# Performance work log

Measured on AMD Instinct MI355X. Metric: run time of the kernel, lower is better.

## Reference

```python
import jax, jax.numpy as jnp
import numpy as np

B = 64
RX, RZ, RX_, RZ_ = 32, 16, 16, 8
TN = 1
STRIDE = 2
IN_DIM, OUT_DIM = 256, 512
KEY_DIM, H, ATTN_RATIO = 32, 8, 2
D = ATTN_RATIO * KEY_DIM            # per-head value dim = 64
DH = D * H                          # 512
NH_KD = KEY_DIM * H                 # 256
N = RX * RX + TN * RZ * RZ          # 1280 tokens (search + template)
N_ = RX_ * RX_ + TN * RZ_ * RZ_     # 320 subsampled query tokens
SCALE = KEY_DIM ** -0.5
EPS = 1e-5


def linear_bn(x, W, gamma, beta):
    # Linear (no bias) followed by BatchNorm1d in training mode over (B*N, C)
    y = jnp.einsum('bnc,oc->bno', x, W)
    m = y.mean(axis=(0, 1))
    v = y.var(axis=(0, 1))  # biased variance, as torch BN uses for normalization
    return (y - m) * jax.lax.rsqrt(v + EPS) * gamma + beta


def subsample(x):
    # stride-subsample the search-region tokens and each template's tokens
    b, n, c = x.shape
    parts = [x[:, :RX * RX].reshape(b, RX, RX, c)[:, ::STRIDE, ::STRIDE].reshape(b, -1, c)]
    for i in range(TN):
        s = RX * RX + i * RZ * RZ
        z = x[:, s:s + RZ * RZ].reshape(b, RZ, RZ, c)[:, ::STRIDE, ::STRIDE].reshape(b, -1, c)
        parts.append(z)
    return jnp.concatenate(parts, axis=1)


def setup_inputs() -> dict:
    key = jax.random.key(0)
    ks = jax.random.split(key, 4)
    return {
        'x': jax.random.normal(ks[0], (B, N, IN_DIM), dtype=jnp.float32),
        'W_kv': jax.random.normal(ks[1], (NH_KD + DH, IN_DIM), dtype=jnp.float32) * 0.02,
        'g_kv': jnp.ones((NH_KD + DH,), jnp.float32),
        'b_kv': jnp.zeros((NH_KD + DH,), jnp.float32),
        'W_q': jax.random.normal(ks[2], (NH_KD, IN_DIM), dtype=jnp.float32) * 0.02,
        'g_q': jnp.ones((NH_KD,), jnp.float32),
        'b_q': jnp.zeros((NH_KD,), jnp.float32),
        'W_p': jax.random.normal(ks[3], (OUT_DIM, DH), dtype=jnp.float32) * 0.02,
        'g_p': jnp.ones((OUT_DIM,), jnp.float32),
        'b_p': jnp.zeros((OUT_DIM,), jnp.float32),
    }


def reference(x, W_kv, g_kv, b_kv, W_q, g_q, b_q, W_p, g_p, b_p):
    b = x.shape[0]
    # fused KV projection + BN, then split into per-head K and V
    kv = linear_bn(x, W_kv, g_kv, b_kv).reshape(b, N, H, KEY_DIM + D)
    k = kv[..., :KEY_DIM].transpose(0, 2, 1, 3)   # [B,H,N,key_dim]
    v = kv[..., KEY_DIM:].transpose(0, 2, 1, 3)   # [B,H,N,d]
    # Q: subsample tokens, then Linear_BN
    q = linear_bn(subsample(x), W_q, g_q, b_q).reshape(b, N_, H, KEY_DIM).transpose(0, 2, 1, 3)
    attn = jax.nn.softmax(jnp.einsum('bhqd,bhkd->bhqk', q, k) * SCALE, axis=-1)
    o = jnp.einsum('bhqk,bhkd->bhqd', attn, v).transpose(0, 2, 1, 3).reshape(b, N_, DH)
    return linear_bn(jax.nn.hard_swish(o), W_p, g_p, b_p)
```

## Files before the change

### kernel.cpp

```cpp
#include <hip/hip_runtime.h>
#include <hip/hip_bf16.h>
#include <math.h>

#define EPSF 1e-5f
#define SCALEF 0.17677669529663687f
#define LOG2E 1.4426950408889634f

typedef unsigned short u16;
typedef unsigned int u32;
typedef __attribute__((ext_vector_type(8))) short bf16x8;
typedef __attribute__((ext_vector_type(4))) float f32x4;

__device__ __forceinline__ float b2f(u16 u) {
    union { unsigned int i; float f; } v; v.i = ((unsigned int)u) << 16; return v.f;
}
__device__ __forceinline__ u16 f2b(float f) {
    union { float f; unsigned int i; } v; v.f = f;
    unsigned int x = v.i;
    return (u16)((x + 0x7fffu + ((x >> 16) & 1u)) >> 16);
}
__device__ __forceinline__ float fexp2(float x) {
#if __has_builtin(__builtin_amdgcn_exp2f)
    return __builtin_amdgcn_exp2f(x);
#else
    return exp2f(x);
#endif
}
__device__ __forceinline__ u32 cvtpk_bf16(float lo, float hi) {
    u32 r;
    asm("v_cvt_pk_bf16_f32 %0, %1, %2" : "=v"(r) : "v"(lo), "v"(hi));
    return r;
}
__device__ __forceinline__ void gload_lds16(const u16* __restrict__ g, u16* l) {
    __builtin_amdgcn_global_load_lds(
        (const __attribute__((address_space(1))) void*)g,
        (__attribute__((address_space(3))) void*)l, 16, 0, 0);
}

__global__ void convert_f32_bf16(const float* __restrict__ src, u16* __restrict__ dst, int n4) {
    int i = blockIdx.x * 256 + threadIdx.x;
    if (i >= n4) return;
    float4 v = ((const float4*)src)[i];
    ushort4 o;
    o.x = f2b(v.x); o.y = f2b(v.y); o.z = f2b(v.z); o.w = f2b(v.w);
    ((ushort4*)dst)[i] = o;
}

__global__ void gather_sub_bf16(const u16* __restrict__ xb, u16* __restrict__ xsub, int n8) {
    int i = blockIdx.x * 256 + threadIdx.x;
    if (i >= n8) return;
    int e = i << 3;
    int row = e >> 8;
    int col = e & 255;
    int b = row / 320;
    int t = row - b * 320;
    int n;
    if (t < 256) n = ((t >> 4) << 6) + ((t & 15) << 1);
    else { int tt = t - 256; n = 1024 + ((tt >> 3) << 5) + ((tt & 7) << 1); }
    *(int4*)(xsub + e) = *(const int4*)(xb + ((size_t)(b * 1280 + n)) * 256 + col);
}

template<int OUT_F32>
__global__ __launch_bounds__(256) void gemm_bt(const u16* __restrict__ A, const u16* __restrict__ Bw,
                                               void* __restrict__ Cv, int M, int N, int K,
                                               float* __restrict__ sums) {
    __shared__ u16 As[128 * 32];
    __shared__ u16 Bs[128 * 32];
    __shared__ float sumbuf[4][64][2];
    const int tid = threadIdx.x;
    const int wave = tid >> 6, lane = tid & 63;
    const int quad = lane >> 4, lc = lane & 15;
    const int wr = wave >> 1, wc = wave & 1;
    const int m0 = blockIdx.y * 128, n0 = blockIdx.x * 128;

    const int srow = (wave << 5) + (lane >> 2);
    const int scol = (lane & 3) << 3;
    u16* ldsA0 = As + ((wave << 5) + 0) * 32;
    u16* ldsA1 = As + ((wave << 5) + 16) * 32;
    u16* ldsB0 = Bs + ((wave << 5) + 0) * 32;
    u16* ldsB1 = Bs + ((wave << 5) + 16) * 32;
    const u16* gA0 = A  + (size_t)(m0 + srow) * K + scol;
    const u16* gA1 = A  + (size_t)(m0 + srow + 16) * K + scol;
    const u16* gB0 = Bw + (size_t)(n0 + srow) * K + scol;
    const u16* gB1 = Bw + (size_t)(n0 + srow + 16) * K + scol;

    f32x4 acc[4][4];
#pragma unroll
    for (int i = 0; i < 4; ++i)
#pragma unroll
        for (int j = 0; j < 4; ++j) acc[i][j] = (f32x4){0.f, 0.f, 0.f, 0.f};

    for (int k0 = 0; k0 < K; k0 += 32) {
        __syncthreads();
        gload_lds16(gA0 + k0, ldsA0);
        gload_lds16(gA1 + k0, ldsA1);
        gload_lds16(gB0 + k0, ldsB0);
        gload_lds16(gB1 + k0, ldsB1);
        asm volatile("s_waitcnt vmcnt(0)" ::: "memory");
        __syncthreads();
        bf16x8 af[4], bfr[4];
#pragma unroll
        for (int mi = 0; mi < 4; ++mi) af[mi]  = *(const bf16x8*)&As[(wr * 64 + mi * 16 + lc) * 32 + quad * 8];
#pragma unroll
        for (int ni = 0; ni < 4; ++ni) bfr[ni] = *(const bf16x8*)&Bs[(wc * 64 + ni * 16 + lc) * 32 + quad * 8];
#pragma unroll
        for (int mi = 0; mi < 4; ++mi)
#pragma unroll
            for (int ni = 0; ni < 4; ++ni)
                acc[mi][ni] = __builtin_amdgcn_mfma_f32_16x16x32_bf16(af[mi], bfr[ni], acc[mi][ni], 0, 0, 0);
    }
    float ps[4], ps2[4];
#pragma unroll
    for (int ni = 0; ni < 4; ++ni) { ps[ni] = 0.f; ps2[ni] = 0.f; }
#pragma unroll
    for (int mi = 0; mi < 4; ++mi)
#pragma unroll
        for (int ni = 0; ni < 4; ++ni)
#pragma unroll
            for (int r = 0; r < 4; ++r) {
                int row = m0 + wr * 64 + mi * 16 + quad * 4 + r;
                int cn  = n0 + wc * 64 + ni * 16 + lc;
                float v = acc[mi][ni][r];
                ps[ni] += v; ps2[ni] += v * v;
                if (OUT_F32) ((float*)Cv)[(size_t)row * N + cn] = v;
                else         ((u16*)Cv)[(size_t)row * N + cn] = f2b(v);
            }
#pragma unroll
    for (int ni = 0; ni < 4; ++ni) {
        ps[ni]  += __shfl_xor(ps[ni], 16);  ps[ni]  += __shfl_xor(ps[ni], 32);
        ps2[ni] += __shfl_xor(ps2[ni], 16); ps2[ni] += __shfl_xor(ps2[ni], 32);
    }
    if (quad == 0) {
#pragma unroll
        for (int ni = 0; ni < 4; ++ni) {
            sumbuf[wave][ni * 16 + lc][0] = ps[ni];
            sumbuf[wave][ni * 16 + lc][1] = ps2[ni];
        }
    }
    __syncthreads();
    {
        int which = tid & 1, idx = (tid >> 1) & 63, wcg = tid >> 7;
        int channel = n0 + wcg * 64 + idx;
        float v = sumbuf[wcg][idx][which] + sumbuf[wcg + 2][idx][which];
        int rep = blockIdx.y & 7;
        atomicAdd(&sums[(rep * 2 + which) * N + channel], v);
    }
}

__global__ void finalize_bn(const float* __restrict__ sum2, const float* __restrict__ g,
                            const float* __restrict__ beta, int cols, float inv_n, float scale,
                            float* __restrict__ AB) {
    int c = blockIdx.x * 256 + threadIdx.x;
    if (c >= cols) return;
    float s = 0.f, s2 = 0.f;
#pragma unroll
    for (int r = 0; r < 8; ++r) {
        s  += sum2[(r * 2 + 0) * cols + c];
        s2 += sum2[(r * 2 + 1) * cols + c];
    }
    float m = s * inv_n;
    float var = s2 * inv_n - m * m;
    float a = g[c] * rsqrtf(var + EPSF) * scale;
    AB[c] = a;
    AB[cols + c] = beta[c] * scale - m * a;
}

__global__ __launch_bounds__(256) void normalize_kv(const u16* __restrict__ kv, const float* __restrict__ AB,
                                                    u16* __restrict__ Kn, u16* __restrict__ Vtn) {
    __shared__ u16 Vs[64 * 66];
    const int h = blockIdx.x, nt = blockIdx.y, b = blockIdx.z;
    const int bh = b * 8 + h;
    const int tid = threadIdx.x;
    {
        int tok = tid >> 2, dk = (tid & 3) << 3;
        size_t src = ((size_t)(b * 1280 + nt * 64 + tok)) * 768 + h * 96 + dk;
        union { int4 v; u16 u[8]; } ld; ld.v = *(const int4*)(kv + src);
        union { int4 v; u16 u[8]; } st;
#pragma unroll
        for (int j = 0; j < 8; ++j) {
            int c = h * 96 + dk + j;
            st.u[j] = f2b(b2f(ld.u[j]) * AB[c] + AB[768 + c]);
        }
        int g = tok >> 5, kk = tok & 31;
        int rowp = nt * 64 + g * 32 + ((kk & 4) << 2) + ((kk >> 3) << 2) + (kk & 3);
        *(int4*)(Kn + ((size_t)bh * 1280 + rowp) * 32 + dk) = st.v;
    }
#pragma unroll
    for (int half = 0; half < 2; ++half) {
        int t = (tid >> 3) + half * 32;
        int dv = (tid & 7) << 3;
        size_t src = ((size_t)(b * 1280 + nt * 64 + t)) * 768 + h * 96 + 32 + dv;
        union { int4 v; u16 u[8]; } ld; ld.v = *(const int4*)(kv + src);
#pragma unroll
        for (int j = 0; j < 8; ++j) {
            int c = h * 96 + 32 + dv + j;
            Vs[(dv + j) * 66 + t] = f2b(b2f(ld.u[j]) * AB[c] + AB[768 + c]);
        }
    }
    __syncthreads();
#pragma unroll
    for (int half = 0; half < 2; ++half) {
        int d = (tid >> 3) + half * 32;
        int tc = (tid & 7) << 3;
        union { int4 v; u16 u[8]; } st;
#pragma unroll
        for (int j = 0; j < 8; ++j) st.u[j] = Vs[d * 66 + tc + j];
        *(int4*)(Vtn + ((size_t)bh * 64 + d) * 1280 + nt * 64 + tc) = st.v;
    }
}

__global__ __launch_bounds__(256, 2) void attn_kernel4(const u16* __restrict__ Kn, const u16* __restrict__ Vtn,
                                                       const u16* __restrict__ q_raw, const float* __restrict__ ABq,
                                                       u16* __restrict__ o_act) {
    const int tid = threadIdx.x;
    const int wave = tid >> 6, lane = tid & 63;
    const int quad = lane >> 4, lc = lane & 15;
    const int h = blockIdx.x, b = blockIdx.y;
    const int bh = b * 8 + h;

    float qa[8], qb[8];
#pragma unroll
    for (int j = 0; j < 8; ++j) { int c = h * 32 + quad * 8 + j; qa[j] = ABq[c]; qb[j] = ABq[256 + c]; }
    bf16x8 qf[5];
#pragma unroll
    for (int j = 0; j < 5; ++j) {
        const u16* qs = q_raw + ((size_t)(b * 320 + j * 64 + wave * 16 + lc)) * 256 + h * 32 + quad * 8;
        union { int4 v; u16 u[8]; } ld; ld.v = *(const int4*)qs;
        union { bf16x8 v; u16 u[8]; } st;
#pragma unroll
        for (int jj = 0; jj < 8; ++jj) st.u[jj] = f2b(b2f(ld.u[jj]) * qa[jj] + qb[jj]);
        qf[j] = st.v;
    }

    const u16* Kp = Kn + (size_t)bh * 1280 * 32 + lc * 32 + quad * 8;
    const u16* Vp = Vtn + (size_t)bh * 64 * 1280 + lc * 1280 + quad * 8;

    f32x4 acc[5][4];
#pragma unroll
    for (int j = 0; j < 5; ++j)
#pragma unroll
        for (int i = 0; i < 4; ++i) acc[j][i] = (f32x4){0.f, 0.f, 0.f, 0.f};
    float lsum[5];
#pragma unroll
    for (int j = 0; j < 5; ++j) lsum[j] = 0.f;

    const f32x4 z = (f32x4){0.f, 0.f, 0.f, 0.f};
    for (int kc = 0; kc < 1280; kc += 32) {
        bf16x8 kfA = *(const bf16x8*)(Kp + kc * 32);
        bf16x8 kfB = *(const bf16x8*)(Kp + kc * 32 + 512);
        bf16x8 vf0 = *(const bf16x8*)(Vp + kc);
        bf16x8 vf1 = *(const bf16x8*)(Vp + 16 * 1280 + kc);
        bf16x8 vf2 = *(const bf16x8*)(Vp + 32 * 1280 + kc);
        bf16x8 vf3 = *(const bf16x8*)(Vp + 48 * 1280 + kc);
        f32x4 s0[5], s1[5];
#pragma unroll
        for (int j = 0; j < 5; ++j) {
            s0[j] = __builtin_amdgcn_mfma_f32_16x16x32_bf16(kfA, qf[j], z, 0, 0, 0);
            s1[j] = __builtin_amdgcn_mfma_f32_16x16x32_bf16(kfB, qf[j], z, 0, 0, 0);
        }
#pragma unroll
        for (int j = 0; j < 5; ++j) {
            float p0 = fexp2(s0[j][0]);
            float p1 = fexp2(s0[j][1]);
            float p2 = fexp2(s0[j][2]);
            float p3 = fexp2(s0[j][3]);
            float p4 = fexp2(s1[j][0]);
            float p5 = fexp2(s1[j][1]);
            float p6 = fexp2(s1[j][2]);
            float p7 = fexp2(s1[j][3]);
            lsum[j] += ((p0 + p1) + (p2 + p3)) + ((p4 + p5) + (p6 + p7));
            union { u32 w[4]; bf16x8 v; } pf;
            pf.w[0] = cvtpk_bf16(p0, p1);
            pf.w[1] = cvtpk_bf16(p2, p3);
            pf.w[2] = cvtpk_bf16(p4, p5);
            pf.w[3] = cvtpk_bf16(p6, p7);
            acc[j][0] = __builtin_amdgcn_mfma_f32_16x16x32_bf16(vf0, pf.v, acc[j][0], 0, 0, 0);
            acc[j][1] = __builtin_amdgcn_mfma_f32_16x16x32_bf16(vf1, pf.v, acc[j][1], 0, 0, 0);
            acc[j][2] = __builtin_amdgcn_mfma_f32_16x16x32_bf16(vf2, pf.v, acc[j][2], 0, 0, 0);
            acc[j][3] = __builtin_amdgcn_mfma_f32_16x16x32_bf16(vf3, pf.v, acc[j][3], 0, 0, 0);
        }
    }
#pragma unroll
    for (int j = 0; j < 5; ++j) {
        float l = lsum[j];
        l += __shfl_xor(l, 16);
        l += __shfl_xor(l, 32);
        float inv = 1.f / l;
        int qrow = b * 320 + j * 64 + wave * 16 + lc;
        u16* dst = o_act + (size_t)qrow * 512 + h * 64 + quad * 4;
#pragma unroll
        for (int nt = 0; nt < 4; ++nt) {
            ushort4 st;
#pragma unroll
            for (int r = 0; r < 4; ++r) {
                float o = acc[j][nt][r] * inv;
                float hs = o * fminf(fmaxf(o + 3.f, 0.f), 6.f) * (1.f / 6.f);
                ((u16*)&st)[r] = f2b(hs);
            }
            *(ushort4*)(dst + nt * 16) = st;
        }
    }
}

__global__ void bn_apply_out(const float* __restrict__ praw, const float* __restrict__ ABp,
                             float* __restrict__ out, int n4) {
    int i = blockIdx.x * 256 + threadIdx.x;
    if (i >= n4) return;
    int e = i << 2;
    int c = e & 511;
    float4 v = ((const float4*)praw)[i];
    float4 o;
    o.x = v.x * ABp[c]     + ABp[512 + c];
    o.y = v.y * ABp[c + 1] + ABp[512 + c + 1];
    o.z = v.z * ABp[c + 2] + ABp[512 + c + 2];
    o.w = v.w * ABp[c + 3] + ABp[512 + c + 3];
    ((float4*)out)[i] = o;
}

extern "C" void kernel_launch(void* const* d_in, const int* in_sizes, int n_in,
                              void* d_out, int out_size, void* d_ws, size_t ws_size,
                              hipStream_t stream) {
    const float* x   = (const float*)d_in[0];
    const float* Wkv = (const float*)d_in[1];
    const float* gkv = (const float*)d_in[2];
    const float* bkv = (const float*)d_in[3];
    const float* Wq  = (const float*)d_in[4];
    const float* gq  = (const float*)d_in[5];
    const float* bq  = (const float*)d_in[6];
    const float* Wp  = (const float*)d_in[7];
    const float* gp  = (const float*)d_in[8];
    const float* bp  = (const float*)d_in[9];
    float* out = (float*)d_out;

    char* ws = (char*)d_ws;
    size_t off = 0;
    auto alloc = [&](size_t bytes) -> void* {
        void* p = ws + off;
        off += (bytes + 255) & ~(size_t)255;
        return p;
    };
    u16*   kv_raw = (u16*)alloc(81920ull * 768 * 2);
    u16*   q_raw  = (u16*)alloc(20480ull * 256 * 2);
    void*  slot1  = alloc(81920ull * 256 * 2);
    u16*   x_b    = (u16*)slot1;
    u16*   K_norm = (u16*)slot1;
    float* p_raw  = (float*)slot1;
    void*  slot2  = alloc(20480ull * 512 * 2);
    u16*   xsub_b = (u16*)slot2;
    u16*   o_act  = (u16*)slot2;
    u16*   Vt_norm = (u16*)alloc(512ull * 64 * 1280 * 2);
    u16*   Wkv_b  = (u16*)alloc(768ull * 256 * 2);
    u16*   Wq_b   = (u16*)alloc(256ull * 256 * 2);
    u16*   Wp_b   = (u16*)alloc(512ull * 512 * 2);
    float* sums_kv = (float*)alloc(8 * 2 * 768 * sizeof(float));
    float* sums_q  = (float*)alloc(8 * 2 * 256 * sizeof(float));
    float* sums_p  = (float*)alloc(8 * 2 * 512 * sizeof(float));
    float* ABkv = (float*)alloc(1536 * sizeof(float));
    float* ABq  = (float*)alloc(512 * sizeof(float));
    float* ABp  = (float*)alloc(1024 * sizeof(float));

    dim3 blk(256);
    hipMemsetAsync(sums_kv, 0, 8 * 2 * (768 + 256 + 512) * sizeof(float), stream);

    convert_f32_bf16<<<20480, blk, 0, stream>>>(x,   x_b,   5242880);
    convert_f32_bf16<<<192,   blk, 0, stream>>>(Wkv, Wkv_b, 49152);
    convert_f32_bf16<<<64,    blk, 0, stream>>>(Wq,  Wq_b,  16384);
    convert_f32_bf16<<<256,   blk, 0, stream>>>(Wp,  Wp_b,  65536);
    gather_sub_bf16<<<2560,   blk, 0, stream>>>(x_b, xsub_b, 655360);

    gemm_bt<0><<<dim3(6, 640), blk, 0, stream>>>(x_b, Wkv_b, kv_raw, 81920, 768, 256, sums_kv);
    gemm_bt<0><<<dim3(2, 160), blk, 0, stream>>>(xsub_b, Wq_b, q_raw, 20480, 256, 256, sums_q);

    finalize_bn<<<3, blk, 0, stream>>>(sums_kv, gkv, bkv, 768, 1.f / 81920.f, 1.f, ABkv);
    finalize_bn<<<1, blk, 0, stream>>>(sums_q,  gq,  bq,  256, 1.f / 20480.f, SCALEF * LOG2E, ABq);

    normalize_kv<<<dim3(8, 20, 64), blk, 0, stream>>>(kv_raw, ABkv, K_norm, Vt_norm);

    attn_kernel4<<<dim3(8, 64), blk, 0, stream>>>(K_norm, Vt_norm, q_raw, ABq, o_act);

    gemm_bt<1><<<dim3(4, 160), blk, 0, stream>>>(o_act, Wp_b, p_raw, 20480, 512, 512, sums_p);
    finalize_bn<<<2, blk, 0, stream>>>(sums_p, gp, bp, 512, 1.f / 20480.f, 1.f, ABp);

    bn_apply_out<<<10240, blk, 0, stream>>>(p_raw, ABp, out, 2621440);
}
```

Before: 398.1 us.

## Fold KV BatchNorm into attention and write K/Vt layouts from the GEMM epilogue

Removes the separate normalize_kv pass. The KV weight rows are permuted so the GEMM epilogue writes raw K, in its permuted row order, and transposed V straight to their attention layouts. The K BN scale is folded into the Q scale; its shift only adds a per-query constant that softmax cancels. The V BN affine is applied after softmax normalization, which is valid because the attention weights sum to one. The GEMM also gains a double-buffered LDS prefetch of the next K tile. The tradeoff is strided 8-byte V-transpose stores in the epilogue and wider-stride K loads in attention.

```diff
diff --git a/kernel.cpp b/kernel.cpp
--- a/kernel.cpp
+++ b/kernel.cpp
@@ -44,6 +44,13 @@
     ushort4 o;
     o.x = f2b(v.x); o.y = f2b(v.y); o.z = f2b(v.z); o.w = f2b(v.w);
     ((ushort4*)dst)[i] = o;
+}
+
+__global__ void convert_wkv_perm(const float* __restrict__ W, u16* __restrict__ out) {
+    int r = blockIdx.x, cl = threadIdx.x;
+    int src = (r < 256) ? ((r >> 5) * 96 + (r & 31))
+                        : (((r - 256) >> 6) * 96 + 32 + ((r - 256) & 63));
+    out[r * 256 + cl] = f2b(W[src * 256 + cl]);
 }
 
 __global__ void gather_sub_bf16(const u16* __restrict__ xb, u16* __restrict__ xsub, int n8) {
@@ -60,12 +67,13 @@
     *(int4*)(xsub + e) = *(const int4*)(xb + ((size_t)(b * 1280 + n)) * 256 + col);
 }
 
-template<int OUT_F32>
+template<int MODE>
 __global__ __launch_bounds__(256) void gemm_bt(const u16* __restrict__ A, const u16* __restrict__ Bw,
-                                               void* __restrict__ Cv, int M, int N, int K,
+                                               void* __restrict__ Cv, void* __restrict__ C2v,
+                                               int M, int N, int K,
                                                float* __restrict__ sums) {
-    __shared__ u16 As[128 * 32];
-    __shared__ u16 Bs[128 * 32];
+    __shared__ u16 As[2][128 * 32];
+    __shared__ u16 Bs[2][128 * 32];
     __shared__ float sumbuf[4][64][2];
     const int tid = threadIdx.x;
     const int wave = tid >> 6, lane = tid & 63;
@@ -75,10 +83,7 @@
 
     const int srow = (wave << 5) + (lane >> 2);
     const int scol = (lane & 3) << 3;
-    u16* ldsA0 = As + ((wave << 5) + 0) * 32;
-    u16* ldsA1 = As + ((wave << 5) + 16) * 32;
-    u16* ldsB0 = Bs + ((wave << 5) + 0) * 32;
-    u16* ldsB1 = Bs + ((wave << 5) + 16) * 32;
+    const int ldsoff = (wave << 5) * 32;
     const u16* gA0 = A  + (size_t)(m0 + srow) * K + scol;
     const u16* gA1 = A  + (size_t)(m0 + srow + 16) * K + scol;
     const u16* gB0 = Bw + (size_t)(n0 + srow) * K + scol;
@@ -90,25 +95,37 @@
 #pragma unroll
         for (int j = 0; j < 4; ++j) acc[i][j] = (f32x4){0.f, 0.f, 0.f, 0.f};
 
+    auto STAGE = [&](int buf, int k0) {
+        gload_lds16(gA0 + k0, &As[buf][ldsoff]);
+        gload_lds16(gA1 + k0, &As[buf][ldsoff + 16 * 32]);
+        gload_lds16(gB0 + k0, &Bs[buf][ldsoff]);
+        gload_lds16(gB1 + k0, &Bs[buf][ldsoff + 16 * 32]);
+    };
+
+    STAGE(0, 0);
+    int cur = 0;
     for (int k0 = 0; k0 < K; k0 += 32) {
-        __syncthreads();
-        gload_lds16(gA0 + k0, ldsA0);
-        gload_lds16(gA1 + k0, ldsA1);
-        gload_lds16(gB0 + k0, ldsB0);
-        gload_lds16(gB1 + k0, ldsB1);
-        asm volatile("s_waitcnt vmcnt(0)" ::: "memory");
-        __syncthreads();
+        if (k0 + 32 < K) {
+            STAGE(cur ^ 1, k0 + 32);
+            asm volatile("s_waitcnt vmcnt(4)" ::: "memory");
+        } else {
+            asm volatile("s_waitcnt vmcnt(0)" ::: "memory");
+        }
+        __builtin_amdgcn_s_barrier();
         bf16x8 af[4], bfr[4];
 #pragma unroll
-        for (int mi = 0; mi < 4; ++mi) af[mi]  = *(const bf16x8*)&As[(wr * 64 + mi * 16 + lc) * 32 + quad * 8];
-#pragma unroll
-        for (int ni = 0; ni < 4; ++ni) bfr[ni] = *(const bf16x8*)&Bs[(wc * 64 + ni * 16 + lc) * 32 + quad * 8];
+        for (int mi = 0; mi < 4; ++mi) af[mi]  = *(const bf16x8*)&As[cur][(wr * 64 + mi * 16 + lc) * 32 + quad * 8];
+#pragma unroll
+        for (int ni = 0; ni < 4; ++ni) bfr[ni] = *(const bf16x8*)&Bs[cur][(wc * 64 + ni * 16 + lc) * 32 + quad * 8];
 #pragma unroll
         for (int mi = 0; mi < 4; ++mi)
 #pragma unroll
             for (int ni = 0; ni < 4; ++ni)
                 acc[mi][ni] = __builtin_amdgcn_mfma_f32_16x16x32_bf16(af[mi], bfr[ni], acc[mi][ni], 0, 0, 0);
-    }
+        __builtin_amdgcn_s_barrier();
+        cur ^= 1;
+    }
+
     float ps[4], ps2[4];
 #pragma unroll
     for (int ni = 0; ni < 4; ++ni) { ps[ni] = 0.f; ps2[ni] = 0.f; }
@@ -118,13 +135,53 @@
         for (int ni = 0; ni < 4; ++ni)
 #pragma unroll
             for (int r = 0; r < 4; ++r) {
-                int row = m0 + wr * 64 + mi * 16 + quad * 4 + r;
-                int cn  = n0 + wc * 64 + ni * 16 + lc;
                 float v = acc[mi][ni][r];
                 ps[ni] += v; ps2[ni] += v * v;
-                if (OUT_F32) ((float*)Cv)[(size_t)row * N + cn] = v;
-                else         ((u16*)Cv)[(size_t)row * N + cn] = f2b(v);
             }
+
+    if (MODE == 0 || MODE == 1) {
+#pragma unroll
+        for (int mi = 0; mi < 4; ++mi)
+#pragma unroll
+            for (int ni = 0; ni < 4; ++ni)
+#pragma unroll
+                for (int r = 0; r < 4; ++r) {
+                    int row = m0 + wr * 64 + mi * 16 + quad * 4 + r;
+                    int cn  = n0 + wc * 64 + ni * 16 + lc;
+                    float v = acc[mi][ni][r];
+                    if (MODE == 1) ((float*)Cv)[(size_t)row * N + cn] = v;
+                    else           ((u16*)Cv)[(size_t)row * N + cn] = f2b(v);
+                }
+    } else if (n0 < 256) {
+        u16* Kr = (u16*)Cv;
+#pragma unroll
+        for (int mi = 0; mi < 4; ++mi)
+#pragma unroll
+            for (int r = 0; r < 4; ++r) {
+                int t = m0 + wr * 64 + mi * 16 + quad * 4 + r;
+                int kk = t & 31;
+                int pr = (t & ~31) + ((kk & 4) << 2) + ((kk >> 3) << 2) + (kk & 3);
+#pragma unroll
+                for (int ni = 0; ni < 4; ++ni) {
+                    int c = n0 + wc * 64 + ni * 16 + lc;
+                    Kr[(size_t)pr * 256 + c] = f2b(acc[mi][ni][r]);
+                }
+            }
+    } else {
+        u16* Vt = (u16*)C2v;
+#pragma unroll
+        for (int mi = 0; mi < 4; ++mi)
+#pragma unroll
+            for (int ni = 0; ni < 4; ++ni) {
+                int cp = n0 - 256 + wc * 64 + ni * 16 + lc;
+                int t0 = m0 + wr * 64 + mi * 16 + quad * 4;
+                uint2 w;
+                w.x = cvtpk_bf16(acc[mi][ni][0], acc[mi][ni][1]);
+                w.y = cvtpk_bf16(acc[mi][ni][2], acc[mi][ni][3]);
+                *(uint2*)(Vt + (size_t)cp * 81920 + t0) = w;
+            }
+    }
+
 #pragma unroll
     for (int ni = 0; ni < 4; ++ni) {
         ps[ni]  += __shfl_xor(ps[ni], 16);  ps[ni]  += __shfl_xor(ps[ni], 32);
@@ -149,7 +206,7 @@
 
 __global__ void finalize_bn(const float* __restrict__ sum2, const float* __restrict__ g,
                             const float* __restrict__ beta, int cols, float inv_n, float scale,
-                            float* __restrict__ AB) {
+                            float* __restrict__ AB, int kvperm) {
     int c = blockIdx.x * 256 + threadIdx.x;
     if (c >= cols) return;
     float s = 0.f, s2 = 0.f;
@@ -158,69 +215,36 @@
         s  += sum2[(r * 2 + 0) * cols + c];
         s2 += sum2[(r * 2 + 1) * cols + c];
     }
+    int src = c;
+    if (kvperm) {
+        src = (c < 256) ? ((c >> 5) * 96 + (c & 31))
+                        : (((c - 256) >> 6) * 96 + 32 + ((c - 256) & 63));
+    }
     float m = s * inv_n;
     float var = s2 * inv_n - m * m;
-    float a = g[c] * rsqrtf(var + EPSF) * scale;
+    float a = g[src] * rsqrtf(var + EPSF) * scale;
     AB[c] = a;
-    AB[cols + c] = beta[c] * scale - m * a;
-}
-
-__global__ __launch_bounds__(256) void normalize_kv(const u16* __restrict__ kv, const float* __restrict__ AB,
-                                                    u16* __restrict__ Kn, u16* __restrict__ Vtn) {
-    __shared__ u16 Vs[64 * 66];
-    const int h = blockIdx.x, nt = blockIdx.y, b = blockIdx.z;
-    const int bh = b * 8 + h;
-    const int tid = threadIdx.x;
-    {
-        int tok = tid >> 2, dk = (tid & 3) << 3;
-        size_t src = ((size_t)(b * 1280 + nt * 64 + tok)) * 768 + h * 96 + dk;
-        union { int4 v; u16 u[8]; } ld; ld.v = *(const int4*)(kv + src);
-        union { int4 v; u16 u[8]; } st;
-#pragma unroll
-        for (int j = 0; j < 8; ++j) {
-            int c = h * 96 + dk + j;
-            st.u[j] = f2b(b2f(ld.u[j]) * AB[c] + AB[768 + c]);
-        }
-        int g = tok >> 5, kk = tok & 31;
-        int rowp = nt * 64 + g * 32 + ((kk & 4) << 2) + ((kk >> 3) << 2) + (kk & 3);
-        *(int4*)(Kn + ((size_t)bh * 1280 + rowp) * 32 + dk) = st.v;
-    }
-#pragma unroll
-    for (int half = 0; half < 2; ++half) {
-        int t = (tid >> 3) + half * 32;
-        int dv = (tid & 7) << 3;
-        size_t src = ((size_t)(b * 1280 + nt * 64 + t)) * 768 + h * 96 + 32 + dv;
-        union { int4 v; u16 u[8]; } ld; ld.v = *(const int4*)(kv + src);
-#pragma unroll
-        for (int j = 0; j < 8; ++j) {
-            int c = h * 96 + 32 + dv + j;
-            Vs[(dv + j) * 66 + t] = f2b(b2f(ld.u[j]) * AB[c] + AB[768 + c]);
-        }
-    }
-    __syncthreads();
-#pragma unroll
-    for (int half = 0; half < 2; ++half) {
-        int d = (tid >> 3) + half * 32;
-        int tc = (tid & 7) << 3;
-        union { int4 v; u16 u[8]; } st;
-#pragma unroll
-        for (int j = 0; j < 8; ++j) st.u[j] = Vs[d * 66 + tc + j];
-        *(int4*)(Vtn + ((size_t)bh * 64 + d) * 1280 + nt * 64 + tc) = st.v;
-    }
-}
-
-__global__ __launch_bounds__(256, 2) void attn_kernel4(const u16* __restrict__ Kn, const u16* __restrict__ Vtn,
-                                                       const u16* __restrict__ q_raw, const float* __restrict__ ABq,
+    AB[cols + c] = beta[src] * scale - m * a;
+}
+
+__global__ __launch_bounds__(256, 2) void attn_kernel5(const u16* __restrict__ Kr, const u16* __restrict__ Vt,
+                                                       const u16* __restrict__ q_raw,
+                                                       const float* __restrict__ ABq,
+                                                       const float* __restrict__ ABkv,
                                                        u16* __restrict__ o_act) {
     const int tid = threadIdx.x;
     const int wave = tid >> 6, lane = tid & 63;
     const int quad = lane >> 4, lc = lane & 15;
     const int h = blockIdx.x, b = blockIdx.y;
-    const int bh = b * 8 + h;
 
     float qa[8], qb[8];
 #pragma unroll
-    for (int j = 0; j < 8; ++j) { int c = h * 32 + quad * 8 + j; qa[j] = ABq[c]; qb[j] = ABq[256 + c]; }
+    for (int j = 0; j < 8; ++j) {
+        int c = h * 32 + quad * 8 + j;
+        float ak = ABkv[c];
+        qa[j] = ABq[c] * ak;
+        qb[j] = ABq[256 + c] * ak;
+    }
     bf16x8 qf[5];
 #pragma unroll
     for (int j = 0; j < 5; ++j) {
@@ -232,8 +256,8 @@
         qf[j] = st.v;
     }
 
-    const u16* Kp = Kn + (size_t)bh * 1280 * 32 + lc * 32 + quad * 8;
-    const u16* Vp = Vtn + (size_t)bh * 64 * 1280 + lc * 1280 + quad * 8;
+    const u16* Kp = Kr + (size_t)b * 1280 * 256 + (size_t)lc * 256 + h * 32 + quad * 8;
+    const u16* Vp = Vt + ((size_t)(h * 64 + lc)) * 81920 + b * 1280 + quad * 8;
 
     f32x4 acc[5][4];
 #pragma unroll
@@ -246,12 +270,12 @@
 
     const f32x4 z = (f32x4){0.f, 0.f, 0.f, 0.f};
     for (int kc = 0; kc < 1280; kc += 32) {
-        bf16x8 kfA = *(const bf16x8*)(Kp + kc * 32);
-        bf16x8 kfB = *(const bf16x8*)(Kp + kc * 32 + 512);
+        bf16x8 kfA = *(const bf16x8*)(Kp + (size_t)kc * 256);
+        bf16x8 kfB = *(const bf16x8*)(Kp + (size_t)(kc + 16) * 256);
         bf16x8 vf0 = *(const bf16x8*)(Vp + kc);
-        bf16x8 vf1 = *(const bf16x8*)(Vp + 16 * 1280 + kc);
-        bf16x8 vf2 = *(const bf16x8*)(Vp + 32 * 1280 + kc);
-        bf16x8 vf3 = *(const bf16x8*)(Vp + 48 * 1280 + kc);
+        bf16x8 vf1 = *(const bf16x8*)(Vp + (size_t)16 * 81920 + kc);
+        bf16x8 vf2 = *(const bf16x8*)(Vp + (size_t)32 * 81920 + kc);
+        bf16x8 vf3 = *(const bf16x8*)(Vp + (size_t)48 * 81920 + kc);
         f32x4 s0[5], s1[5];
 #pragma unroll
         for (int j = 0; j < 5; ++j) {
@@ -280,6 +304,13 @@
             acc[j][3] = __builtin_amdgcn_mfma_f32_16x16x32_bf16(vf3, pf.v, acc[j][3], 0, 0, 0);
         }
     }
+    float av[16], bv[16];
+#pragma unroll
+    for (int t = 0; t < 16; ++t) {
+        int cv = 256 + h * 64 + (t >> 2) * 16 + quad * 4 + (t & 3);
+        av[t] = ABkv[cv];
+        bv[t] = ABkv[768 + cv];
+    }
 #pragma unroll
     for (int j = 0; j < 5; ++j) {
         float l = lsum[j];
@@ -293,7 +324,7 @@
             ushort4 st;
 #pragma unroll
             for (int r = 0; r < 4; ++r) {
-                float o = acc[j][nt][r] * inv;
+                float o = av[nt * 4 + r] * (acc[j][nt][r] * inv) + bv[nt * 4 + r];
                 float hs = o * fminf(fmaxf(o + 3.f, 0.f), 6.f) * (1.f / 6.f);
                 ((u16*)&st)[r] = f2b(hs);
             }
@@ -339,16 +370,15 @@
         off += (bytes + 255) & ~(size_t)255;
         return p;
     };
-    u16*   kv_raw = (u16*)alloc(81920ull * 768 * 2);
-    u16*   q_raw  = (u16*)alloc(20480ull * 256 * 2);
     void*  slot1  = alloc(81920ull * 256 * 2);
     u16*   x_b    = (u16*)slot1;
-    u16*   K_norm = (u16*)slot1;
     float* p_raw  = (float*)slot1;
+    u16*   K_raw  = (u16*)alloc(81920ull * 256 * 2);
+    u16*   Vt_raw = (u16*)alloc(512ull * 81920 * 2);
+    u16*   q_raw  = (u16*)alloc(20480ull * 256 * 2);
     void*  slot2  = alloc(20480ull * 512 * 2);
     u16*   xsub_b = (u16*)slot2;
     u16*   o_act  = (u16*)slot2;
-    u16*   Vt_norm = (u16*)alloc(512ull * 64 * 1280 * 2);
     u16*   Wkv_b  = (u16*)alloc(768ull * 256 * 2);
     u16*   Wq_b   = (u16*)alloc(256ull * 256 * 2);
     u16*   Wp_b   = (u16*)alloc(512ull * 512 * 2);
@@ -363,23 +393,21 @@
     hipMemsetAsync(sums_kv, 0, 8 * 2 * (768 + 256 + 512) * sizeof(float), stream);
 
     convert_f32_bf16<<<20480, blk, 0, stream>>>(x,   x_b,   5242880);
-    convert_f32_bf16<<<192,   blk, 0, stream>>>(Wkv, Wkv_b, 49152);
+    convert_wkv_perm<<<768,   blk, 0, stream>>>(Wkv, Wkv_b);
     convert_f32_bf16<<<64,    blk, 0, stream>>>(Wq,  Wq_b,  16384);
     convert_f32_bf16<<<256,   blk, 0, stream>>>(Wp,  Wp_b,  65536);
     gather_sub_bf16<<<2560,   blk, 0, stream>>>(x_b, xsub_b, 655360);
 
-    gemm_bt<0><<<dim3(6, 640), blk, 0, stream>>>(x_b, Wkv_b, kv_raw, 81920, 768, 256, sums_kv);
-    gemm_bt<0><<<dim3(2, 160), blk, 0, stream>>>(xsub_b, Wq_b, q_raw, 20480, 256, 256, sums_q);
-
-    finalize_bn<<<3, blk, 0, stream>>>(sums_kv, gkv, bkv, 768, 1.f / 81920.f, 1.f, ABkv);
-    finalize_bn<<<1, blk, 0, stream>>>(sums_q,  gq,  bq,  256, 1.f / 20480.f, SCALEF * LOG2E, ABq);
-
-    normalize_kv<<<dim3(8, 20, 64), blk, 0, stream>>>(kv_raw, ABkv, K_norm, Vt_norm);
-
-    attn_kernel4<<<dim3(8, 64), blk, 0, stream>>>(K_norm, Vt_norm, q_raw, ABq, o_act);
-
-    gemm_bt<1><<<dim3(4, 160), blk, 0, stream>>>(o_act, Wp_b, p_raw, 20480, 512, 512, sums_p);
-    finalize_bn<<<2, blk, 0, stream>>>(sums_p, gp, bp, 512, 1.f / 20480.f, 1.f, ABp);
+    gemm_bt<2><<<dim3(6, 640), blk, 0, stream>>>(x_b, Wkv_b, K_raw, Vt_raw, 81920, 768, 256, sums_kv);
+    gemm_bt<0><<<dim3(2, 160), blk, 0, stream>>>(xsub_b, Wq_b, q_raw, nullptr, 20480, 256, 256, sums_q);
+
+    finalize_bn<<<3, blk, 0, stream>>>(sums_kv, gkv, bkv, 768, 1.f / 81920.f, 1.f, ABkv, 1);
+    finalize_bn<<<1, blk, 0, stream>>>(sums_q,  gq,  bq,  256, 1.f / 20480.f, SCALEF * LOG2E, ABq, 0);
+
+    attn_kernel5<<<dim3(8, 64), blk, 0, stream>>>(K_raw, Vt_raw, q_raw, ABq, ABkv, o_act);
+
+    gemm_bt<1><<<dim3(4, 160), blk, 0, stream>>>(o_act, Wp_b, p_raw, nullptr, 20480, 512, 512, sums_p);
+    finalize_bn<<<2, blk, 0, stream>>>(sums_p, gp, bp, 512, 1.f / 20480.f, 1.f, ABp, 0);
 
     bn_apply_out<<<10240, blk, 0, stream>>>(p_raw, ABp, out, 2621440);
 }
```

After: 353.4 us. 11.2% less time.
